# Kernel tuning notes

Measured on AMD Instinct MI355X. Metric: run time of the kernel, lower is better.

## Reference

```python
import jax, jax.numpy as jnp
import numpy as np

B, T, R, A = 4, 40, 2000, 36864
H = W = 64
C = 256
PP = 7
RED = 16.0
NCLS = 21
NPOS = 64   # rois_per_image*B//4
NNEG = 192  # rois_per_image*B*3//4
DH = 1024

def _iou(b1, b2):
    # boxes are (top,left,bottom,right)
    t = jnp.maximum(b1[..., 0], b2[..., 0])
    l = jnp.maximum(b1[..., 1], b2[..., 1])
    b = jnp.minimum(b1[..., 2], b2[..., 2])
    r = jnp.minimum(b1[..., 3], b2[..., 3])
    inter = jnp.clip(b - t, 0.0) * jnp.clip(r - l, 0.0)
    a1 = (b1[..., 2] - b1[..., 0]) * (b1[..., 3] - b1[..., 1])
    a2 = (b2[..., 2] - b2[..., 0]) * (b2[..., 3] - b2[..., 1])
    return inter / (a1 + a2 - inter)

def _smooth_l1(p, t):
    d = jnp.abs(p - t)
    return jnp.mean(jnp.where(d < 1.0, 0.5 * d * d, d - 0.5))

def _roi_pool(fm, rois):
    # fm [B,C,H,W], rois [N,5] = (img_id, top,left,bottom,right) in feature-map coords
    fmt = jnp.transpose(fm, (0, 2, 3, 1))  # [B,H,W,C]
    n = rois[:, 0].astype(jnp.int32)[:, None, None]
    t, l, b, r = rois[:, 1], rois[:, 2], rois[:, 3], rois[:, 4]
    g = (jnp.arange(PP, dtype=fm.dtype) + 0.5) / PP
    ys = jnp.clip(t[:, None] + g * (b - t)[:, None], 0.0, H - 1.0)
    xs = jnp.clip(l[:, None] + g * (r - l)[:, None], 0.0, W - 1.0)
    y0 = jnp.floor(ys).astype(jnp.int32)
    x0 = jnp.floor(xs).astype(jnp.int32)
    y1 = jnp.minimum(y0 + 1, H - 1)
    x1 = jnp.minimum(x0 + 1, W - 1)
    wy = (ys - y0)[:, :, None, None]
    wx = (xs - x0)[:, None, :, None]
    def gat(yi, xi):
        return fmt[n, yi[:, :, None], xi[:, None, :], :]  # [N,PP,PP,C]
    v = (gat(y0, x0) * (1 - wy) * (1 - wx) + gat(y0, x1) * (1 - wy) * wx
         + gat(y1, x0) * wy * (1 - wx) + gat(y1, x1) * wy * wx)
    return v.reshape(v.shape[0], -1)  # [N, PP*PP*C]

def _forward(nms_reg, nms_cls, feature_maps, bboxes, classes, anchors, rpn_reg, rpn_cls, W1, b1, Wr, br, Wc, bc):
    # ---------------- RPN trainer: anchor/target matching ----------------
    iou_a = _iou(bboxes[:, :, None, :], anchors[None, None, :, :])   # [B,T,A]
    max_iou = jnp.max(iou_a, axis=1)                                  # [B,A]
    tidx = jnp.argmax(iou_a, axis=1)
    max_tgt = jnp.take_along_axis(bboxes, jnp.broadcast_to(tidx[:, :, None], (B, A, 4)), axis=1)
    mask = (max_iou > 0.5).reshape(-1)
    pos = jnp.nonzero(mask, size=128)[0]        # first 128 positives, flat order (matches cls[mask][:128])
    neg = jnp.nonzero(~mask, size=256 - B)[0]   # torch quirk: 256 - len(mask_matched) = 256 - B
    clsf = rpn_cls.reshape(-1)
    logits = jnp.concatenate([clsf[pos], clsf[neg]])
    lbl = jnp.concatenate([jnp.ones(128, dtype=logits.dtype), jnp.zeros(256 - B, dtype=logits.dtype)])
    rpn_cls_loss = jnp.mean(jnp.maximum(logits, 0) - logits * lbl + jnp.log1p(jnp.exp(-jnp.abs(logits))))
    anc_f = jnp.broadcast_to(anchors[None], (B, A, 4)).reshape(-1, 4)
    rpn_reg_loss = _smooth_l1(rpn_reg.reshape(-1, 4)[pos], max_tgt.reshape(-1, 4)[pos] - anc_f[pos]) / 4.0

    # ------------- RCNN trainer: proposal matching + sampling -------------
    iou_r = _iou(nms_reg[:, None, :, :], bboxes[:, :, None, :])  # [B,T,R]
    iou_m = jnp.max(iou_r, axis=1)                               # [B,R]
    ridx = jnp.argmax(iou_r, axis=1)
    iou_f = iou_m.reshape(-1)
    posr = jnp.nonzero(iou_f > 0.5, size=NPOS)[0]                # first NPOS positives, flat order
    negscore = jnp.where(iou_f <= 0.5, iou_f, -jnp.inf)
    negr = jax.lax.top_k(negscore, NNEG)[1]                      # negatives sorted by IoU descending
    cls_g = jnp.take_along_axis(classes, ridx, axis=1).reshape(-1)
    cls_s = jnp.concatenate([cls_g[posr], jnp.zeros(NNEG, dtype=cls_g.dtype)])
    imid = jnp.repeat(jnp.arange(B, dtype=nms_reg.dtype), R)
    nmsf = nms_reg.reshape(-1, 4)
    sel = jnp.concatenate([posr, negr])
    rois = jnp.concatenate([imid[sel][:, None], nmsf[sel]], axis=1)  # [256,5]
    feat = _roi_pool(feature_maps, rois)
    hmid = jax.nn.relu(feat @ W1 + b1)
    rreg = hmid @ Wr + br
    rcls = hmid @ Wc + bc
    logp = jax.nn.log_softmax(rcls, axis=-1)
    rcnn_cls_loss = -jnp.mean(jnp.take_along_axis(logp, cls_s[:, None], axis=1))
    posb = nmsf[posr]
    rounded = jnp.concatenate([jnp.floor(posb[:, :2] * RED), jnp.ceil(posb[:, 2:] * RED)], axis=1) / RED
    mb = jnp.take_along_axis(bboxes, jnp.broadcast_to(ridx[:, :, None], (B, R, 4)), axis=1).reshape(-1, 4)[posr]
    tgt = mb - rounded
    pr = rreg[:NPOS]
    rcnn_reg_loss = sum(_smooth_l1(pr[:, c], tgt[:, c]) for c in range(4)) / 4.0
    offset = sum(jnp.mean(jnp.abs(pr[:, c] - tgt[:, c])) for c in range(4)) / 4.0
    acc = jnp.mean((jnp.argmax(rcls[:NPOS], axis=-1) == cls_s[:NPOS]).astype(jnp.float32))
    return rpn_cls_loss, rpn_reg_loss, rcnn_cls_loss, rcnn_reg_loss, acc, offset

def _boxes(k, shape):
    k1, k2 = jax.random.split(k)
    c = jax.random.uniform(k1, shape + (2,), minval=10.0, maxval=54.0)
    h = jax.random.uniform(k2, shape + (2,), minval=3.0, maxval=8.0)
    return jnp.concatenate([c - h, c + h], axis=-1)  # (top,left,bottom,right)

def setup_inputs():
    key = jax.random.key(0)
    ks = jax.random.split(key, 13)
    base = _boxes(ks[0], (T,))
    shift = jax.random.uniform(ks[1], (B, T, 2), minval=-0.2, maxval=0.2)
    bboxes = base[None] + jnp.concatenate([shift, shift], axis=-1)  # guarantees >=128 RPN positives
    classes = jax.random.randint(ks[2], (B, T), 1, NCLS)
    anchors = _boxes(ks[3], (A,)).at[:T].set(base)
    nms_reg = _boxes(ks[4], (B, R))
    shift2 = jax.random.uniform(ks[5], (B, T, 2), minval=-0.1, maxval=0.1)
    nms_reg = nms_reg.at[:, :T].set(bboxes + jnp.concatenate([shift2, shift2], axis=-1))  # >=64 RCNN positives
    nms_cls = jax.random.normal(ks[6], (B, R))
    feature_maps = jax.random.normal(ks[7], (B, C, H, W))
    rpn_reg = 0.1 * jax.random.normal(ks[8], (B, A, 4))
    rpn_cls = jax.random.normal(ks[9], (B, A))
    D = PP * PP * C
    W1 = jax.random.normal(ks[10], (D, DH)) * float(1.0 / np.sqrt(D))
    b1 = jnp.zeros((DH,))
    Wr = jax.random.normal(ks[11], (DH, 4)) * float(1.0 / np.sqrt(DH))
    br = jnp.zeros((4,))
    Wc = jax.random.normal(ks[12], (DH, NCLS)) * float(1.0 / np.sqrt(DH))
    bc = jnp.zeros((NCLS,))
    return dict(nms_reg=nms_reg, nms_cls=nms_cls, feature_maps=feature_maps, bboxes=bboxes,
                classes=classes, anchors=anchors, rpn_reg=rpn_reg, rpn_cls=rpn_cls,
                W1=W1, b1=b1, Wr=Wr, br=br, Wc=Wc, bc=bc)

def reference(nms_reg, nms_cls, feature_maps, bboxes, classes, anchors, rpn_reg, rpn_cls, W1, b1, Wr, br, Wc, bc):
    return _forward(nms_reg, nms_cls, feature_maps, bboxes, classes, anchors, rpn_reg, rpn_cls, W1, b1, Wr, br, Wc, bc)
```

## Files before the change

### kernel.cpp

```cpp
#include <hip/hip_runtime.h>

typedef unsigned short u16;
typedef unsigned long long u64;

constexpr int cB = 4, cT = 40, cR = 2000, cA = 36864;
constexpr int cH = 64, cW = 64, cC = 256, cPP = 7;
constexpr int cNCLS = 21, cNPOS = 64, cNNEG = 192, cDH = 1024;
constexpr int cD = cPP * cPP * cC;
constexpr int cBA = cB * cA;
constexpr int cBR = cB * cR;
constexpr int NW64 = cBA / 64;
constexpr int SPLITS = 8;
constexpr int KCH = cD / SPLITS;
constexpr unsigned POSKEY = 0x007FFFFFu;

constexpr size_t O_TIDX  = 0;
constexpr size_t O_MASKW = (size_t)cBA * 4;
constexpr size_t O_FMT   = 0;
constexpr size_t O_CPART = 0;
constexpr size_t O_PERS  = 8388608;
constexpr size_t O_SEL   = O_PERS;
constexpr size_t O_CLS   = O_PERS + 1024;
constexpr size_t O_ROIS  = O_PERS + 2048;
constexpr size_t O_TGT   = O_PERS + 6144;
constexpr size_t O_FEAT  = O_PERS + 8192;
constexpr size_t O_RREG  = O_FEAT + (size_t)256 * cD * 2;
constexpr size_t O_RCLS  = O_RREG + 4096;
constexpr size_t O_KEYS  = O_RCLS + 24576;
constexpr size_t O_RIDXG = O_KEYS + 32000;

__device__ __forceinline__ float b2f(u16 u) {
  return __uint_as_float(((unsigned)u) << 16);
}
__device__ __forceinline__ u16 f2b(float f) {
  unsigned x = __float_as_uint(f);
  unsigned r = x + 0x7FFFu + ((x >> 16) & 1u);
  return (u16)(r >> 16);
}
__device__ __forceinline__ unsigned f2key(float f) {
  unsigned b = __float_as_uint(f);
  return b ^ ((b & 0x80000000u) ? 0xFFFFFFFFu : 0x80000000u);
}

typedef __attribute__((ext_vector_type(8))) short short8;
typedef __attribute__((ext_vector_type(4))) float f32x4;

__global__ void k_ious(const float* __restrict__ bboxes, const float* __restrict__ anchors,
                       const float* __restrict__ nms_reg,
                       int* __restrict__ tidx, u64* __restrict__ maskw,
                       unsigned* __restrict__ keys, int* __restrict__ ridxg) {
  __shared__ float sb[cB * cT * 4];
  if (blockIdx.x < 576) {
    int b = blockIdx.x / 144;
    if (threadIdx.x < cT * 4) sb[threadIdx.x] = bboxes[b * cT * 4 + threadIdx.x];
    __syncthreads();
    int i = blockIdx.x * 256 + threadIdx.x;
    int a = i - b * cA;
    float4 av = ((const float4*)anchors)[a];
    float at = av.x, al = av.y, ab = av.z, ar = av.w;
    float area_a = (ab - at) * (ar - al);
    float best = -1.0f; int bi = 0;
    for (int t = 0; t < cT; ++t) {
      float bt = sb[t * 4], bl = sb[t * 4 + 1], bbv = sb[t * 4 + 2], brv = sb[t * 4 + 3];
      float ih = fmaxf(fminf(bbv, ab) - fmaxf(bt, at), 0.0f);
      float iw = fmaxf(fminf(brv, ar) - fmaxf(bl, al), 0.0f);
      float inter = ih * iw;
      float a1 = (bbv - bt) * (brv - bl);
      float iou = inter / (a1 + area_a - inter);
      if (iou > best) { best = iou; bi = t; }
    }
    tidx[i] = bi;
    u64 bal = __ballot(best > 0.5f);
    if ((threadIdx.x & 63) == 0) maskw[i >> 6] = bal;
  } else {
    for (int j = threadIdx.x; j < cB * cT * 4; j += 256) sb[j] = bboxes[j];
    __syncthreads();
    int i = (blockIdx.x - 576) * 256 + threadIdx.x;
    if (i >= cBR) return;
    int b = i / cR;
    float4 nv = ((const float4*)nms_reg)[i];
    float nt = nv.x, nl = nv.y, nb = nv.z, nr = nv.w;
    float area_n = (nb - nt) * (nr - nl);
    float best = -1.0f; int bi = 0;
    for (int t = 0; t < cT; ++t) {
      const float* bx = &sb[(b * cT + t) * 4];
      float ih = fmaxf(fminf(bx[2], nb) - fmaxf(bx[0], nt), 0.0f);
      float iw = fmaxf(fminf(bx[3], nr) - fmaxf(bx[1], nl), 0.0f);
      float inter = ih * iw;
      float a1 = (bx[2] - bx[0]) * (bx[3] - bx[1]);
      float iou = inter / (a1 + area_n - inter);
      if (iou > best) { best = iou; bi = t; }
    }
    keys[i] = (best <= 0.5f) ? f2key(best) : POSKEY;
    ridxg[i] = bi;
  }
}

__global__ __launch_bounds__(1024) void k_select(
    const u64* __restrict__ maskw, const int* __restrict__ tidx,
    const float* __restrict__ rpn_cls, const float* __restrict__ rpn_reg,
    const float* __restrict__ bboxes, const float* __restrict__ anchors,
    const unsigned* __restrict__ keysg, const int* __restrict__ ridxg,
    const float* __restrict__ nms_reg, const int* __restrict__ classes,
    int* __restrict__ sel, int* __restrict__ cls_s,
    float* __restrict__ rois, float* __restrict__ tgt,
    float* __restrict__ out) {
  __shared__ __align__(16) char smem[50688];
  __shared__ float s_scalF[2];
  __shared__ int s_scalI[3];
  int tid = threadIdx.x, lane = tid & 63, w = tid >> 6;
  u64 lmask = (1ULL << lane) - 1ULL;

  if (blockIdx.x == 0) {
    u64* s_w   = (u64*)smem;
    int* s_pre = (int*)(smem + 18432);
    int* s_cw  = (int*)(smem + 19008);
    int* s_pos = (int*)(smem + 19584);
    int* s_neg = (int*)(smem + 20096);
    for (int k = tid; k < NW64; k += 1024) s_w[k] = maskw[k];
    if (tid < 128) s_pos[tid] = 0;
    if (tid < 252) s_neg[tid] = 0;
    if (tid == 0) { s_scalF[0] = 0.0f; s_scalF[1] = 0.0f; }
    __syncthreads();
    if (tid < 144) {
      int c = 0;
      #pragma unroll
      for (int k2 = 0; k2 < 16; ++k2) c += __popcll(s_w[tid * 16 + k2]);
      s_cw[tid] = c;
    }
    __syncthreads();
    if (tid == 0) {
      int run = 0;
      for (int ch = 0; ch < 144; ++ch) { s_pre[ch] = run; run += s_cw[ch]; }
    }
    __syncthreads();
    for (int ch = w; ch < 144; ch += 16) {
      int pbase = s_pre[ch];
      int nbase = ch * 1024 - pbase;
      if (pbase >= 128 && nbase >= 252) continue;
      int pc = 0;
      #pragma unroll
      for (int s2 = 0; s2 < 16; ++s2) {
        u64 word = s_w[ch * 16 + s2];
        bool m = (word >> lane) & 1ULL;
        int prefP = __popcll(word & lmask);
        int idx = ch * 1024 + s2 * 64 + lane;
        if (m) {
          int g = pbase + pc + prefP;
          if (g < 128) s_pos[g] = idx;
        } else {
          int g = nbase + (s2 * 64 + lane) - (pc + prefP);
          if (g < 252) s_neg[g] = idx;
        }
        pc += __popcll(word);
      }
    }
    __syncthreads();
    if (tid < 380) {
      int flat; float lbl;
      if (tid < 128) { flat = s_pos[tid]; lbl = 1.0f; }
      else           { flat = s_neg[tid - 128]; lbl = 0.0f; }
      float l = rpn_cls[flat];
      float term = fmaxf(l, 0.0f) - l * lbl + log1pf(expf(-fabsf(l)));
      atomicAdd(&s_scalF[0], term);
    }
    if (tid < 512) {
      int j = tid >> 2, c = tid & 3;
      int flat = s_pos[j];
      int b = flat / cA, a = flat - b * cA;
      int t = tidx[flat];
      float p = rpn_reg[flat * 4 + c];
      float tg = bboxes[(b * cT + t) * 4 + c] - anchors[a * 4 + c];
      float d = fabsf(p - tg);
      float sl = (d < 1.0f) ? 0.5f * d * d : d - 0.5f;
      atomicAdd(&s_scalF[1], sl);
    }
    __syncthreads();
    if (tid == 0) {
      out[0] = s_scalF[0] / 380.0f;
      out[1] = s_scalF[1] / 512.0f / 4.0f;
    }
  } else {
    unsigned* s_key = (unsigned*)smem;
    int* s_hist = (int*)(smem + 32000);
    int* s_pc   = (int*)(smem + 48384);
    int* s_wsum = (int*)(smem + 48896);
    int* s_wsuf = (int*)(smem + 48960);
    int* s_posr = (int*)(smem + 49024);
    int* s_negr = (int*)(smem + 49280);

    for (int i = tid; i < cBR; i += 1024) s_key[i] = keysg[i];
    if (tid < 64) s_posr[tid] = 0;
    __syncthreads();

    {
      int myv = 0; int mypre[8];
      #pragma unroll
      for (int p = 0; p < 8; ++p) {
        int i = p * 1024 + tid;
        bool v = (i < cBR) && (s_key[i] == POSKEY);
        u64 bal = __ballot(v);
        if (lane == 0) s_pc[p * 16 + w] = __popcll(bal);
        mypre[p] = __popcll(bal & lmask);
        myv |= v ? (1 << p) : 0;
      }
      __syncthreads();
      if (tid == 0) {
        int run = 0;
        for (int k = 0; k < 128; ++k) { int t = s_pc[k]; s_pc[k] = run; run += t; }
      }
      __syncthreads();
      #pragma unroll
      for (int p = 0; p < 8; ++p) {
        if (myv & (1 << p)) {
          int g = s_pc[p * 16 + w] + mypre[p];
          if (g < 64) s_posr[g] = p * 1024 + tid;
        }
      }
    }

    unsigned thr = 0; int G = 0;
    int need = cNNEG;
    #pragma unroll
    for (int lvl = 0; lvl < 3; ++lvl) {
      __syncthreads();
      #pragma unroll
      for (int k = 0; k < 4; ++k) s_hist[tid * 4 + k] = 0;
      __syncthreads();
      #pragma unroll
      for (int p = 0; p < 8; ++p) {
        int i = p * 1024 + tid;
        if (i < cBR) {
          unsigned key = s_key[i];
          int bkt = -1;
          if (lvl == 0) bkt = key >> 20;
          else if (lvl == 1) { if ((key >> 20) == (thr >> 20)) bkt = (key >> 8) & 0xFFF; }
          else { if ((key >> 8) == (thr >> 8)) bkt = (key & 0xFF) << 4; }
          if (bkt >= 0) atomicAdd(&s_hist[bkt], 1);
        }
      }
      __syncthreads();
      int local0 = s_hist[tid * 4 + 0], local1 = s_hist[tid * 4 + 1];
      int local2 = s_hist[tid * 4 + 2], local3 = s_hist[tid * 4 + 3];
      int lsum = local0 + local1 + local2 + local3;
      int x = lsum;
      #pragma unroll
      for (int off = 1; off < 64; off <<= 1) {
        int t = __shfl_down(x, off, 64);
        if (lane + off < 64) x += t;
      }
      if (lane == 0) s_wsum[w] = x;
      __syncthreads();
      if (tid == 0) {
        int run = 0;
        for (int wi = 15; wi >= 0; --wi) { s_wsuf[wi] = run; run += s_wsum[wi]; }
      }
      __syncthreads();
      int above = s_wsuf[w] + (x - lsum);
      int run = above;
      int loc[4] = {local3, local2, local1, local0};
      #pragma unroll
      for (int j = 0; j < 4; ++j) {
        int S = run + loc[j];
        if (run < need && S >= need) { s_scalI[0] = tid * 4 + (3 - j); s_scalI[1] = run; }
        run = S;
      }
      __syncthreads();
      int bS = s_scalI[0], ov = s_scalI[1];
      if (lvl == 0) thr = ((unsigned)bS) << 20;
      else if (lvl == 1) thr |= ((unsigned)bS) << 8;
      else thr |= ((unsigned)bS) >> 4;
      G += ov;
      need -= ov;
    }

    if (tid == 0) s_scalI[2] = 0;
    __syncthreads();
    #pragma unroll
    for (int p = 0; p < 8; ++p) {
      int i = p * 1024 + tid;
      if (i < cBR && s_key[i] > thr) {
        int slot = atomicAdd(&s_scalI[2], 1);
        s_negr[slot] = i;
      }
    }
    {
      __syncthreads();
      int myv = 0; int mypre[8];
      #pragma unroll
      for (int p = 0; p < 8; ++p) {
        int i = p * 1024 + tid;
        bool v = (i < cBR) && (s_key[i] == thr);
        u64 bal = __ballot(v);
        if (lane == 0) s_pc[p * 16 + w] = __popcll(bal);
        mypre[p] = __popcll(bal & lmask);
        myv |= v ? (1 << p) : 0;
      }
      __syncthreads();
      if (tid == 0) {
        int run = 0;
        for (int k = 0; k < 128; ++k) { int t = s_pc[k]; s_pc[k] = run; run += t; }
      }
      __syncthreads();
      #pragma unroll
      for (int p = 0; p < 8; ++p) {
        if (myv & (1 << p)) {
          int g = s_pc[p * 16 + w] + mypre[p];
          if (g < need) s_negr[G + g] = p * 1024 + tid;
        }
      }
    }
    __syncthreads();

    if (tid < 256) {
      int flat = (tid < 64) ? s_posr[tid] : s_negr[tid - 64];
      sel[tid] = flat;
      int b = flat / cR;
      #pragma unroll
      for (int c = 0; c < 4; ++c) rois[tid * 4 + c] = nms_reg[flat * 4 + c];
      cls_s[tid] = (tid < 64) ? classes[b * cT + ridxg[flat]] : 0;
      if (tid < 64) {
        int mt = ridxg[flat];
        #pragma unroll
        for (int c = 0; c < 4; ++c) {
          float v = nms_reg[flat * 4 + c];
          float rr = ((c < 2) ? floorf(v * 16.0f) : ceilf(v * 16.0f)) / 16.0f;
          float mbv = bboxes[(b * cT + mt) * 4 + c];
          tgt[tid * 4 + c] = mbv - rr;
        }
      }
    }
  }
}

__global__ __launch_bounds__(256) void k_fmt(const float* __restrict__ fm, u16* __restrict__ fmt) {
  __shared__ float tile[64][65];
  int b = blockIdx.z;
  int p0 = blockIdx.x * 64, c0 = blockIdx.y * 64;
  int t = threadIdx.x;
  int pL = (t & 15) * 4, cL = t >> 4;
  #pragma unroll
  for (int i = 0; i < 4; ++i) {
    int c = cL + i * 16;
    float4 v = *(const float4*)&fm[((size_t)b * cC + c0 + c) * (cH * cW) + p0 + pL];
    tile[c][pL] = v.x; tile[c][pL + 1] = v.y; tile[c][pL + 2] = v.z; tile[c][pL + 3] = v.w;
  }
  __syncthreads();
  int pW = t >> 2, cg = (t & 3) * 16;
  unsigned pk[8];
  #pragma unroll
  for (int j = 0; j < 8; ++j) {
    unsigned lo = f2b(tile[cg + 2 * j][pW]);
    unsigned hi = f2b(tile[cg + 2 * j + 1][pW]);
    pk[j] = lo | (hi << 16);
  }
  u16* dst = &fmt[((size_t)b * (cH * cW) + p0 + pW) * cC + c0 + cg];
  *(uint4*)dst = *(uint4*)&pk[0];
  *(uint4*)(dst + 8) = *(uint4*)&pk[4];
}

__global__ void k_roi_pool(const u16* __restrict__ fmt, const float* __restrict__ rois,
                           const int* __restrict__ sel, u16* __restrict__ feat) {
  int j = blockIdx.x;
  int py = blockIdx.y;
  int c = threadIdx.x;
  int flat = sel[j];
  int n = flat / cR;
  float t = rois[j * 4 + 0], l = rois[j * 4 + 1];
  float bb = rois[j * 4 + 2], r = rois[j * 4 + 3];
  const u16* base = fmt + (size_t)n * (cH * cW) * cC;
  float gy = (py + 0.5f) / (float)cPP;
  float ys = fminf(fmaxf(t + gy * (bb - t), 0.0f), 63.0f);
  int y0 = (int)floorf(ys);
  int y1 = min(y0 + 1, 63);
  float wy = ys - (float)y0;
  #pragma unroll
  for (int px = 0; px < cPP; ++px) {
    float gx = (px + 0.5f) / (float)cPP;
    float xs = fminf(fmaxf(l + gx * (r - l), 0.0f), 63.0f);
    int x0 = (int)floorf(xs);
    int x1 = min(x0 + 1, 63);
    float wx = xs - (float)x0;
    float f00 = b2f(base[(y0 * cW + x0) * cC + c]);
    float f01 = b2f(base[(y0 * cW + x1) * cC + c]);
    float f10 = b2f(base[(y1 * cW + x0) * cC + c]);
    float f11 = b2f(base[(y1 * cW + x1) * cC + c]);
    float v = f00 * (1.0f - wy) * (1.0f - wx) + f01 * (1.0f - wy) * wx +
              f10 * wy * (1.0f - wx) + f11 * wy * wx;
    feat[((size_t)j * 49 + py * cPP + px) * cC + c] = f2b(v);
  }
}

__global__ __launch_bounds__(256) void k_gemm1(const u16* __restrict__ feat, const float* __restrict__ W1,
                                               float* __restrict__ Cpart) {
  __shared__ u16 As[64][56];
  __shared__ u16 Bs[64][56];
  int tid = threadIdx.x;
  int n0 = blockIdx.x * 64;
  int kb0 = blockIdx.y * KCH;
  int m0 = blockIdx.z * 64;
  int lane = tid & 63, w = tid >> 6;
  int r = lane & 15, q = lane >> 4;
  f32x4 acc[4] = {};
  int arow = tid >> 2, ak = (tid & 3) * 8;
  int bk = tid >> 3, bn = (tid & 7) * 8;
  uint4 ra;
  float4 rb0, rb1;
  {
    ra = *(const uint4*)&feat[(size_t)(m0 + arow) * cD + kb0 + ak];
    const float* bp = &W1[(size_t)(kb0 + bk) * cDH + n0 + bn];
    rb0 = *(const float4*)bp; rb1 = *(const float4*)(bp + 4);
  }
  for (int kc = 0; kc < KCH / 32; ++kc) {
    __syncthreads();
    *(uint4*)&As[arow][ak] = ra;
    {
      float bv[8] = {rb0.x, rb0.y, rb0.z, rb0.w, rb1.x, rb1.y, rb1.z, rb1.w};
      int kg = bk >> 3, kw = bk & 7;
      #pragma unroll
      for (int i = 0; i < 8; ++i) {
        int row = bn + i;
        Bs[row][((kg ^ ((row >> 3) & 3)) << 3) + kw] = f2b(bv[i]);
      }
    }
    if (kc + 1 < KCH / 32) {
      int kb = kb0 + (kc + 1) * 32;
      ra = *(const uint4*)&feat[(size_t)(m0 + arow) * cD + kb + ak];
      const float* bp = &W1[(size_t)(kb + bk) * cDH + n0 + bn];
      rb0 = *(const float4*)bp; rb1 = *(const float4*)(bp + 4);
    }
    __syncthreads();
    short8 a = *(const short8*)&As[w * 16 + r][q * 8];
    #pragma unroll
    for (int nt = 0; nt < 4; ++nt) {
      int n = nt * 16 + r;
      short8 bfr = *(const short8*)&Bs[n][(q ^ ((n >> 3) & 3)) << 3];
      acc[nt] = __builtin_amdgcn_mfma_f32_16x16x32_bf16(a, bfr, acc[nt], 0, 0, 0);
    }
  }
  float* Cp = Cpart + (size_t)blockIdx.y * 256 * cDH;
  #pragma unroll
  for (int nt = 0; nt < 4; ++nt) {
    #pragma unroll
    for (int rg = 0; rg < 4; ++rg) {
      int row = m0 + w * 16 + q * 4 + rg;
      int col = n0 + nt * 16 + r;
      Cp[(size_t)row * cDH + col] = acc[nt][rg];
    }
  }
}

__global__ void k_heads(const float* __restrict__ Cpart, const float* __restrict__ b1,
                        const float* __restrict__ Wr, const float* __restrict__ br,
                        const float* __restrict__ Wc, const float* __restrict__ bc,
                        float* __restrict__ rreg, float* __restrict__ rcls) {
  int w = threadIdx.x >> 6, lane = threadIdx.x & 63;
  int row = blockIdx.x * 4 + w;
  float part[25];
  #pragma unroll
  for (int c = 0; c < 25; ++c) part[c] = 0.0f;
  for (int k = lane; k < cDH; k += 64) {
    float h = b1[k];
    #pragma unroll
    for (int s = 0; s < SPLITS; ++s) h += Cpart[(size_t)s * 256 * cDH + (size_t)row * cDH + k];
    h = fmaxf(h, 0.0f);
    #pragma unroll
    for (int c = 0; c < 4; ++c) part[c] += h * Wr[k * 4 + c];
    #pragma unroll
    for (int c = 0; c < 21; ++c) part[4 + c] += h * Wc[k * 21 + c];
  }
  #pragma unroll
  for (int off = 32; off; off >>= 1) {
    #pragma unroll
    for (int c = 0; c < 25; ++c) part[c] += __shfl_down(part[c], off, 64);
  }
  if (lane == 0) {
    #pragma unroll
    for (int c = 0; c < 4; ++c) rreg[row * 4 + c] = part[c] + br[c];
    #pragma unroll
    for (int c = 0; c < 21; ++c) rcls[row * 21 + c] = part[4 + c] + bc[c];
  }
}

__global__ void k_final(const float* __restrict__ rcls, const float* __restrict__ rreg,
                        const int* __restrict__ cls_s, const float* __restrict__ tgt,
                        float* __restrict__ out) {
  __shared__ float s_cls, s_acc, s_sl1, s_off;
  int tid = threadIdx.x;
  if (tid == 0) { s_cls = 0.0f; s_acc = 0.0f; s_sl1 = 0.0f; s_off = 0.0f; }
  __syncthreads();
  {
    int row = tid;
    float m = -INFINITY;
    for (int c = 0; c < cNCLS; ++c) m = fmaxf(m, rcls[row * cNCLS + c]);
    float sum = 0.0f;
    for (int c = 0; c < cNCLS; ++c) sum += expf(rcls[row * cNCLS + c] - m);
    float lse = m + logf(sum);
    float closs = lse - rcls[row * cNCLS + cls_s[row]];
    atomicAdd(&s_cls, closs);
  }
  if (tid < 64) {
    int am = 0; float bv = rcls[tid * cNCLS];
    for (int c = 1; c < cNCLS; ++c) {
      float v = rcls[tid * cNCLS + c];
      if (v > bv) { bv = v; am = c; }
    }
    if (am == cls_s[tid]) atomicAdd(&s_acc, 1.0f);
    float sl = 0.0f, of = 0.0f;
    #pragma unroll
    for (int c = 0; c < 4; ++c) {
      float d = fabsf(rreg[tid * 4 + c] - tgt[tid * 4 + c]);
      sl += (d < 1.0f) ? 0.5f * d * d : d - 0.5f;
      of += d;
    }
    atomicAdd(&s_sl1, sl);
    atomicAdd(&s_off, of);
  }
  __syncthreads();
  if (tid == 0) {
    out[2] = s_cls / 256.0f;
    out[3] = s_sl1 / 256.0f;
    out[4] = s_acc / 64.0f;
    out[5] = s_off / 256.0f;
  }
}

extern "C" void kernel_launch(void* const* d_in, const int* in_sizes, int n_in,
                              void* d_out, int out_size, void* d_ws, size_t ws_size,
                              hipStream_t stream) {
  const float* nms_reg = (const float*)d_in[0];
  const float* fm      = (const float*)d_in[2];
  const float* bboxes  = (const float*)d_in[3];
  const int*   classes = (const int*)d_in[4];
  const float* anchors = (const float*)d_in[5];
  const float* rpn_reg = (const float*)d_in[6];
  const float* rpn_cls = (const float*)d_in[7];
  const float* W1      = (const float*)d_in[8];
  const float* b1      = (const float*)d_in[9];
  const float* Wr      = (const float*)d_in[10];
  const float* br      = (const float*)d_in[11];
  const float* Wc      = (const float*)d_in[12];
  const float* bc      = (const float*)d_in[13];
  float* out = (float*)d_out;
  char* ws = (char*)d_ws;

  int*      tidx  = (int*)(ws + O_TIDX);
  u64*      maskw = (u64*)(ws + O_MASKW);
  u16*      fmt   = (u16*)(ws + O_FMT);
  float*    Cpart = (float*)(ws + O_CPART);
  int*      sel   = (int*)(ws + O_SEL);
  int*      clss  = (int*)(ws + O_CLS);
  float*    rois  = (float*)(ws + O_ROIS);
  float*    tgt   = (float*)(ws + O_TGT);
  u16*      feat  = (u16*)(ws + O_FEAT);
  float*    rreg  = (float*)(ws + O_RREG);
  float*    rcls  = (float*)(ws + O_RCLS);
  unsigned* keys  = (unsigned*)(ws + O_KEYS);
  int*      ridxg = (int*)(ws + O_RIDXG);

  k_ious<<<576 + 32, 256, 0, stream>>>(bboxes, anchors, nms_reg, tidx, maskw, keys, ridxg);
  k_select<<<2, 1024, 0, stream>>>(maskw, tidx, rpn_cls, rpn_reg, bboxes, anchors,
                                   keys, ridxg, nms_reg, classes, sel, clss, rois, tgt, out);
  k_fmt<<<dim3(cH * cW / 64, cC / 64, cB), 256, 0, stream>>>(fm, fmt);
  k_roi_pool<<<dim3(256, cPP), 256, 0, stream>>>(fmt, rois, sel, feat);
  k_gemm1<<<dim3(16, SPLITS, 4), 256, 0, stream>>>(feat, W1, Cpart);
  k_heads<<<64, 256, 0, stream>>>(Cpart, b1, Wr, br, Wc, bc, rreg, rcls);
  k_final<<<1, 256, 0, stream>>>(rcls, rreg, clss, tgt, out);
}
```

Baseline: 201.0 us.

## Narrow GEMM N-tile, double-buffer prefetch, and parallelize heads per row

The first FC GEMM now uses 64x32 tiles instead of 64x64, which doubles the grid to 1024 blocks. Its register prefetch is two chunks deep, alternating between two buffers, and the swizzled B stores are replaced by a padded transposed layout written with 8-byte stores. The heads kernel now gives each 256-row block its own row, with each thread handling 4 hidden units, and reduces through warp shuffles plus shared-memory atomics. The aim is more parallelism and more latency hiding for the W1 stream. The cost is that A tiles are loaded twice as often and W1 loads are strided scalar reads.

```diff
diff --git a/kernel.cpp b/kernel.cpp
--- a/kernel.cpp
+++ b/kernel.cpp
@@ -12,6 +12,7 @@
 constexpr int NW64 = cBA / 64;
 constexpr int SPLITS = 8;
 constexpr int KCH = cD / SPLITS;
+constexpr int NCH = KCH / 32;
 constexpr unsigned POSKEY = 0x007FFFFFu;
 
 constexpr size_t O_TIDX  = 0;
@@ -393,54 +394,54 @@
 
 __global__ __launch_bounds__(256) void k_gemm1(const u16* __restrict__ feat, const float* __restrict__ W1,
                                                float* __restrict__ Cpart) {
-  __shared__ u16 As[64][56];
-  __shared__ u16 Bs[64][56];
+  __shared__ u16 As[64][40];
+  __shared__ u16 Bs[32][40];
   int tid = threadIdx.x;
-  int n0 = blockIdx.x * 64;
+  int n0 = blockIdx.x * 32;
   int kb0 = blockIdx.y * KCH;
   int m0 = blockIdx.z * 64;
   int lane = tid & 63, w = tid >> 6;
   int r = lane & 15, q = lane >> 4;
-  f32x4 acc[4] = {};
-  int arow = tid >> 2, ak = (tid & 3) * 8;
-  int bk = tid >> 3, bn = (tid & 7) * 8;
-  uint4 ra;
-  float4 rb0, rb1;
-  {
-    ra = *(const uint4*)&feat[(size_t)(m0 + arow) * cD + kb0 + ak];
-    const float* bp = &W1[(size_t)(kb0 + bk) * cDH + n0 + bn];
-    rb0 = *(const float4*)bp; rb1 = *(const float4*)(bp + 4);
-  }
-  for (int kc = 0; kc < KCH / 32; ++kc) {
-    __syncthreads();
-    *(uint4*)&As[arow][ak] = ra;
-    {
-      float bv[8] = {rb0.x, rb0.y, rb0.z, rb0.w, rb1.x, rb1.y, rb1.z, rb1.w};
-      int kg = bk >> 3, kw = bk & 7;
-      #pragma unroll
-      for (int i = 0; i < 8; ++i) {
-        int row = bn + i;
-        Bs[row][((kg ^ ((row >> 3) & 3)) << 3) + kw] = f2b(bv[i]);
-      }
-    }
-    if (kc + 1 < KCH / 32) {
-      int kb = kb0 + (kc + 1) * 32;
-      ra = *(const uint4*)&feat[(size_t)(m0 + arow) * cD + kb + ak];
-      const float* bp = &W1[(size_t)(kb + bk) * cDH + n0 + bn];
-      rb0 = *(const float4*)bp; rb1 = *(const float4*)(bp + 4);
-    }
+  f32x4 acc[2] = {};
+  int arow = tid >> 2, ako = (tid & 3) * 8;
+  int bn2 = tid & 31, bkq = tid >> 5;
+
+  uint4 rA0, rA1;
+  float rb0[4], rb1[4];
+  auto loadAB = [&](int kc, uint4& ra, float* rb) {
+    int kb = kb0 + kc * 32;
+    ra = *(const uint4*)&feat[(size_t)(m0 + arow) * cD + kb + ako];
+    const float* bp = &W1[(size_t)(kb + bkq * 4) * cDH + n0 + bn2];
+    rb[0] = bp[0]; rb[1] = bp[cDH]; rb[2] = bp[2 * cDH]; rb[3] = bp[3 * cDH];
+  };
+  auto step = [&](int kc, uint4& ra, float* rb, bool pf) {
+    __syncthreads();
+    *(uint4*)&As[arow][ako] = ra;
+    union { u16 u[4]; uint2 v; } pb;
+    #pragma unroll
+    for (int j = 0; j < 4; ++j) pb.u[j] = f2b(rb[j]);
+    *(uint2*)&Bs[bn2][bkq * 4] = pb.v;
+    if (pf) loadAB(kc + 2, ra, rb);
     __syncthreads();
     short8 a = *(const short8*)&As[w * 16 + r][q * 8];
     #pragma unroll
-    for (int nt = 0; nt < 4; ++nt) {
-      int n = nt * 16 + r;
-      short8 bfr = *(const short8*)&Bs[n][(q ^ ((n >> 3) & 3)) << 3];
+    for (int nt = 0; nt < 2; ++nt) {
+      short8 bfr = *(const short8*)&Bs[nt * 16 + r][q * 8];
       acc[nt] = __builtin_amdgcn_mfma_f32_16x16x32_bf16(a, bfr, acc[nt], 0, 0, 0);
     }
-  }
+  };
+
+  loadAB(0, rA0, rb0);
+  loadAB(1, rA1, rb1);
+  for (int kc = 0; kc < NCH - 1; kc += 2) {
+    step(kc, rA0, rb0, kc + 2 < NCH);
+    step(kc + 1, rA1, rb1, kc + 3 < NCH);
+  }
+  step(NCH - 1, rA0, rb0, false);
+
   float* Cp = Cpart + (size_t)blockIdx.y * 256 * cDH;
   #pragma unroll
-  for (int nt = 0; nt < 4; ++nt) {
+  for (int nt = 0; nt < 2; ++nt) {
     #pragma unroll
     for (int rg = 0; rg < 4; ++rg) {
       int row = m0 + w * 16 + q * 4 + rg;
@@ -450,24 +451,34 @@
   }
 }
 
-__global__ void k_heads(const float* __restrict__ Cpart, const float* __restrict__ b1,
-                        const float* __restrict__ Wr, const float* __restrict__ br,
-                        const float* __restrict__ Wc, const float* __restrict__ bc,
-                        float* __restrict__ rreg, float* __restrict__ rcls) {
-  int w = threadIdx.x >> 6, lane = threadIdx.x & 63;
-  int row = blockIdx.x * 4 + w;
+__global__ __launch_bounds__(256) void k_heads(
+    const float* __restrict__ Cpart, const float* __restrict__ b1,
+    const float* __restrict__ Wr, const float* __restrict__ br,
+    const float* __restrict__ Wc, const float* __restrict__ bc,
+    float* __restrict__ rreg, float* __restrict__ rcls) {
+  __shared__ float sacc[25];
+  int row = blockIdx.x, tid = threadIdx.x, lane = tid & 63;
+  if (tid < 25) sacc[tid] = 0.0f;
+  __syncthreads();
+  int k0 = tid * 4;
+  float4 h = *(const float4*)&b1[k0];
+  #pragma unroll
+  for (int s = 0; s < SPLITS; ++s) {
+    float4 c = *(const float4*)&Cpart[(size_t)s * 256 * cDH + (size_t)row * cDH + k0];
+    h.x += c.x; h.y += c.y; h.z += c.z; h.w += c.w;
+  }
+  float hv[4] = {fmaxf(h.x, 0.f), fmaxf(h.y, 0.f), fmaxf(h.z, 0.f), fmaxf(h.w, 0.f)};
   float part[25];
   #pragma unroll
   for (int c = 0; c < 25; ++c) part[c] = 0.0f;
-  for (int k = lane; k < cDH; k += 64) {
-    float h = b1[k];
-    #pragma unroll
-    for (int s = 0; s < SPLITS; ++s) h += Cpart[(size_t)s * 256 * cDH + (size_t)row * cDH + k];
-    h = fmaxf(h, 0.0f);
-    #pragma unroll
-    for (int c = 0; c < 4; ++c) part[c] += h * Wr[k * 4 + c];
-    #pragma unroll
-    for (int c = 0; c < 21; ++c) part[4 + c] += h * Wc[k * 21 + c];
+  #pragma unroll
+  for (int j = 0; j < 4; ++j) {
+    float4 wr = *(const float4*)&Wr[(k0 + j) * 4];
+    part[0] += hv[j] * wr.x; part[1] += hv[j] * wr.y;
+    part[2] += hv[j] * wr.z; part[3] += hv[j] * wr.w;
+    const float* wc = &Wc[(k0 + j) * 21];
+    #pragma unroll
+    for (int c = 0; c < 21; ++c) part[4 + c] += hv[j] * wc[c];
   }
   #pragma unroll
   for (int off = 32; off; off >>= 1) {
@@ -476,10 +487,11 @@
   }
   if (lane == 0) {
     #pragma unroll
-    for (int c = 0; c < 4; ++c) rreg[row * 4 + c] = part[c] + br[c];
-    #pragma unroll
-    for (int c = 0; c < 21; ++c) rcls[row * 21 + c] = part[4 + c] + bc[c];
-  }
+    for (int c = 0; c < 25; ++c) atomicAdd(&sacc[c], part[c]);
+  }
+  __syncthreads();
+  if (tid < 4) rreg[row * 4 + tid] = sacc[tid] + br[tid];
+  else if (tid < 25) rcls[row * 21 + (tid - 4)] = sacc[tid] + bc[tid - 4];
 }
 
 __global__ void k_final(const float* __restrict__ rcls, const float* __restrict__ rreg,
@@ -563,7 +575,7 @@
                                    keys, ridxg, nms_reg, classes, sel, clss, rois, tgt, out);
   k_fmt<<<dim3(cH * cW / 64, cC / 64, cB), 256, 0, stream>>>(fm, fmt);
   k_roi_pool<<<dim3(256, cPP), 256, 0, stream>>>(fmt, rois, sel, feat);
-  k_gemm1<<<dim3(16, SPLITS, 4), 256, 0, stream>>>(feat, W1, Cpart);
-  k_heads<<<64, 256, 0, stream>>>(Cpart, b1, Wr, br, Wc, bc, rreg, rcls);
+  k_gemm1<<<dim3(32, SPLITS, 4), 256, 0, stream>>>(feat, W1, Cpart);
+  k_heads<<<256, 256, 0, stream>>>(Cpart, b1, Wr, br, Wc, bc, rreg, rcls);
   k_final<<<1, 256, 0, stream>>>(rcls, rreg, clss, tgt, out);
 }
```

New measurement: 201.3 us. Within noise of the previous version (+0.1%).
